# Performance work log

Hardware: AMD Instinct MI355X
Metric: run time of the kernel (lower is better)

## Reference

```python
import jax, jax.numpy as jnp
import numpy as np

HEAD_DIM = 16

def setup_inputs() -> dict:
    key = jax.random.key(0)
    ks = jax.random.split(key, 6)
    b, m, n, e, k, d = 2, 2048, 2048, 128, 8, HEAD_DIM
    # xavier-uniform-like scale for [e, d] fan
    s = float(np.sqrt(6.0 / (e + d)))
    return {
        "x": jax.random.normal(ks[0], (b, m, e), dtype=jnp.float32),
        "y": jax.random.normal(ks[1], (b, n, e), dtype=jnp.float32),
        "lambda1": jax.random.uniform(ks[2], (k, e, d), jnp.float32, -s, s),
        "lambda2": jax.random.uniform(ks[3], (k, e, d), jnp.float32, -s, s),
        "theta1": jax.random.uniform(ks[4], (k, e, d), jnp.float32, -s, s),
        "theta2": jax.random.uniform(ks[5], (k, e, d), jnp.float32, -s, s),
        "bias_lambda": jnp.zeros((k, d), jnp.float32),
        "bias_theta": jnp.zeros((k, d), jnp.float32),
    }

def reference(x, y, lambda1, lambda2, theta1, theta2, bias_lambda, bias_theta):
    head_dim = lambda1.shape[-1]
    # r: [b, m, k, d]
    r = jnp.einsum('bmp,kpd->bmkd', x, lambda1) + bias_lambda
    # dot_att: [k, b, m, n] (bilinear QK via per-head projections of x and y)
    dot_att = jnp.einsum('bmkd,kqd,bnq->kbmn', r, lambda2, y)
    dot_att = dot_att * (head_dim ** -0.5)
    # softmax over the query/m axis (-2), NOT the key axis
    att = jax.nn.softmax(dot_att, axis=-2)
    # combine: [b, n, k, d]
    r2 = jnp.einsum('kbmn,bmp,kpd->bnkd', att, x, theta1) + bias_theta
    # output: [b, n, emb_dim_x]
    return jnp.einsum('bnkd,kqd->bnq', r2, theta2)
```

## Files before the change

kernel.cpp:

```cpp
#include <hip/hip_runtime.h>
#include <math.h>

#define BB 2
#define MM 2048
#define NN 2048
#define EE 128
#define KH 8
#define DD 16
#define NHEADS (BB * KH)
#define MSPLIT 8
#define MCHUNK (MM / MSPLIT)
#define LOG2E 1.44269504088896340736f
#define QSCALE (0.25f * LOG2E)


typedef __bf16 bf16x8 __attribute__((ext_vector_type(8)));
typedef __bf16 bf16x4 __attribute__((ext_vector_type(4)));
typedef float  f32x16 __attribute__((ext_vector_type(16)));
typedef float  f32x4  __attribute__((ext_vector_type(4)));

__device__ inline bf16x8 cvt8(float4 a, float4 b) {
    bf16x8 r;
    r[0] = (__bf16)a.x; r[1] = (__bf16)a.y; r[2] = (__bf16)a.z; r[3] = (__bf16)a.w;
    r[4] = (__bf16)b.x; r[5] = (__bf16)b.y; r[6] = (__bf16)b.z; r[7] = (__bf16)b.w;
    return r;
}

__global__ __launch_bounds__(256) void proj_kernel(
    const float* __restrict__ x, const float* __restrict__ y,
    const float* __restrict__ lambda1, const float* __restrict__ lambda2,
    const float* __restrict__ theta1, const float* __restrict__ bias_lambda,
    __bf16* __restrict__ rK, __bf16* __restrict__ kyQ, __bf16* __restrict__ Vt)
{
    const int grp  = blockIdx.x;
    const int f    = blockIdx.y;
    const int head = blockIdx.z;
    const int b = head >> 3, kh = head & 7;
    const int wave = threadIdx.x >> 6;
    const int lane = threadIdx.x & 63;
    const int l15 = lane & 15, g4 = lane >> 4;

    const float* W   = ((f == 0) ? lambda1 : (f == 1) ? theta1 : lambda2)
                       + (size_t)kh * EE * DD;
    const float* src = ((f == 2) ? y : x) + (size_t)b * MM * EE;

    bf16x8 wf[4];
    #pragma unroll
    for (int kb = 0; kb < 4; ++kb) {
        const float* wp = W + (size_t)(32 * kb + 8 * g4) * DD + l15;
        bf16x8 t;
        #pragma unroll
        for (int e = 0; e < 8; ++e) t[e] = (__bf16)wp[e * DD];
        wf[kb] = t;
    }
    const float bl = (f == 0) ? bias_lambda[kh * DD + l15] : 0.f;

    const int m0 = (grp * 4 + wave) * 16;
    const float* xp = src + (size_t)(m0 + l15) * EE + 8 * g4;

    f32x4 acc;
    #pragma unroll
    for (int r = 0; r < 4; ++r) acc[r] = 0.f;

    #pragma unroll
    for (int kb = 0; kb < 4; ++kb) {
        float4 a = *(const float4*)(xp + 32 * kb);
        float4 c = *(const float4*)(xp + 32 * kb + 4);
        bf16x8 xf = cvt8(a, c);
        if (f == 1) acc = __builtin_amdgcn_mfma_f32_16x16x32_bf16(wf[kb], xf, acc, 0, 0, 0);
        else        acc = __builtin_amdgcn_mfma_f32_16x16x32_bf16(xf, wf[kb], acc, 0, 0, 0);
    }

    if (f == 0) {
        #pragma unroll
        for (int r = 0; r < 4; ++r)
            rK[((size_t)head * MM + m0 + 4 * g4 + r) * DD + l15] = (__bf16)(acc[r] + bl);
    } else if (f == 2) {
        #pragma unroll
        for (int r = 0; r < 4; ++r)
            kyQ[((size_t)head * NN + m0 + 4 * g4 + r) * DD + l15] = (__bf16)(acc[r] * QSCALE);
    } else {
        #pragma unroll
        for (int r = 0; r < 4; ++r)
            Vt[((size_t)head * DD + 4 * g4 + r) * MM + m0 + l15] = (__bf16)acc[r];
    }
}

__global__ __launch_bounds__(256) void attn_kernel(
    const __bf16* __restrict__ rK, const __bf16* __restrict__ kyQ,
    const __bf16* __restrict__ Vt,
    float* __restrict__ Opart, float* __restrict__ mlP)
{
    __shared__ __bf16 Pst[4][32][40];

    const int tid  = threadIdx.x;
    const int wave = tid >> 6;
    const int lane = tid & 63;
    const int head = blockIdx.x >> 4;
    const int nbase = (blockIdx.x & 15) * 128 + wave * 32;
    const int ms   = blockIdx.y;
    const int b = head >> 3, kh = head & 7;

    const int l31 = lane & 31;
    const int hi  = lane >> 5;
    const int l15 = lane & 15;
    const int g4  = lane >> 4;

    const bf16x8 qf = *reinterpret_cast<const bf16x8*>(
        kyQ + ((size_t)head * NN + nbase + l31) * DD + 8 * hi);

    f32x4 o0, o1;
    #pragma unroll
    for (int i = 0; i < 4; ++i) { o0[i] = 0.f; o1[i] = 0.f; }
    float lsum = 0.f;

    const __bf16* kb = rK + (size_t)head * MM * DD;
    const __bf16* vb = Vt + (size_t)head * DD * MM;

    #pragma unroll
    for (int it = 0; it < MCHUNK / 32; ++it) {
        const int m0 = ms * MCHUNK + it * 32;

        const bf16x8 kf = *reinterpret_cast<const bf16x8*>(
            kb + ((size_t)(m0 + l31)) * DD + 8 * hi);
        const bf16x8 vf = *reinterpret_cast<const bf16x8*>(
            vb + (size_t)l15 * MM + m0 + 8 * g4);

        f32x16 s;
        #pragma unroll
        for (int i = 0; i < 16; ++i) s[i] = 0.f;
        s = __builtin_amdgcn_mfma_f32_32x32x16_bf16(kf, qf, s, 0, 0, 0);

        #pragma unroll
        for (int r = 0; r < 16; ++r) { s[r] = exp2f(s[r]); lsum += s[r]; }

        #pragma unroll
        for (int qd = 0; qd < 4; ++qd) {
            bf16x4 pk;
            pk[0] = (__bf16)s[4 * qd + 0];
            pk[1] = (__bf16)s[4 * qd + 1];
            pk[2] = (__bf16)s[4 * qd + 2];
            pk[3] = (__bf16)s[4 * qd + 3];
            *reinterpret_cast<bf16x4*>(&Pst[wave][l31][8 * qd + 4 * hi]) = pk;
        }

        const bf16x8 pa0 = *reinterpret_cast<const bf16x8*>(&Pst[wave][l15][8 * g4]);
        const bf16x8 pa1 = *reinterpret_cast<const bf16x8*>(&Pst[wave][16 + l15][8 * g4]);

        o0 = __builtin_amdgcn_mfma_f32_16x16x32_bf16(pa0, vf, o0, 0, 0, 0);
        o1 = __builtin_amdgcn_mfma_f32_16x16x32_bf16(pa1, vf, o1, 0, 0, 0);
    }

    lsum += __shfl_xor(lsum, 32);

    float* obase = Opart + (((size_t)ms * BB + b) * NN) * (KH * DD) + kh * DD;
    #pragma unroll
    for (int r = 0; r < 4; ++r) {
        const int n0 = nbase + 4 * g4 + r;
        const int n1 = n0 + 16;
        obase[(size_t)n0 * (KH * DD) + l15] = o0[r];
        obase[(size_t)n1 * (KH * DD) + l15] = o1[r];
    }
    if (lane < 32) {
        mlP[(((size_t)ms * BB + b) * NN + nbase + l31) * KH + kh] = lsum;
    }
}

__global__ __launch_bounds__(256) void combine_kernel(
    const float* __restrict__ Opart, const float* __restrict__ mlP,
    const float* __restrict__ bias_theta, const float* __restrict__ theta2,
    float* __restrict__ out)
{
    __shared__ float r2s[4][128];

    const int blk = blockIdx.x;
    const int b   = blk >> 9;
    const int n0  = (blk & 511) * 4;
    const int tid = threadIdx.x;

    {
        const int n_loc = tid >> 6;
        const int k  = (tid >> 3) & 7;
        const int dh = tid & 7;
        const int n = n0 + n_loc;

        float L = 0.f;
        float2 O = make_float2(0.f, 0.f);
        #pragma unroll
        for (int s = 0; s < MSPLIT; ++s) {
            L += mlP[(((size_t)s * BB + b) * NN + n) * KH + k];
            const float2 op = *(const float2*)(
                Opart + (((size_t)s * BB + b) * NN + n) * (KH * DD) + k * DD + dh * 2);
            O.x += op.x;
            O.y += op.y;
        }
        const float inv = 1.f / L;
        const float* bt = bias_theta + k * DD + dh * 2;
        float2 res;
        res.x = fmaf(O.x, inv, bt[0]);
        res.y = fmaf(O.y, inv, bt[1]);
        *(float2*)&r2s[n_loc][k * DD + dh * 2] = res;
    }
    __syncthreads();
    {
        const int q   = tid & 127;
        const int nl0 = tid >> 7;
        float acc0 = 0.f, acc1 = 0.f;
        #pragma unroll
        for (int k = 0; k < KH; ++k) {
            const float4* t2 = (const float4*)(theta2 + ((size_t)k * EE + q) * DD);
            const float4* ra = (const float4*)&r2s[nl0][k * DD];
            const float4* rb = (const float4*)&r2s[nl0 + 2][k * DD];
            #pragma unroll
            for (int j = 0; j < 4; ++j) {
                const float4 t = t2[j];
                const float4 a = ra[j];
                const float4 bq = rb[j];
                acc0 = fmaf(a.x, t.x, acc0);  acc0 = fmaf(a.y, t.y, acc0);
                acc0 = fmaf(a.z, t.z, acc0);  acc0 = fmaf(a.w, t.w, acc0);
                acc1 = fmaf(bq.x, t.x, acc1); acc1 = fmaf(bq.y, t.y, acc1);
                acc1 = fmaf(bq.z, t.z, acc1); acc1 = fmaf(bq.w, t.w, acc1);
            }
        }
        out[((size_t)b * NN + n0 + nl0) * EE + q]     = acc0;
        out[((size_t)b * NN + n0 + nl0 + 2) * EE + q] = acc1;
    }
}

extern "C" void kernel_launch(void* const* d_in, const int* in_sizes, int n_in,
                              void* d_out, int out_size, void* d_ws, size_t ws_size,
                              hipStream_t stream) {
    const float* x           = (const float*)d_in[0];
    const float* y           = (const float*)d_in[1];
    const float* lambda1     = (const float*)d_in[2];
    const float* lambda2     = (const float*)d_in[3];
    const float* theta1      = (const float*)d_in[4];
    const float* theta2      = (const float*)d_in[5];
    const float* bias_lambda = (const float*)d_in[6];
    const float* bias_theta  = (const float*)d_in[7];
    float* out = (float*)d_out;

    char* w = (char*)d_ws;
    __bf16* rK  = (__bf16*)w;  w += (size_t)NHEADS * MM * DD * 2;
    __bf16* kyQ = (__bf16*)w;  w += (size_t)NHEADS * NN * DD * 2;
    __bf16* Vt  = (__bf16*)w;  w += (size_t)NHEADS * DD * MM * 2;
    float* Opart = (float*)w;  w += (size_t)MSPLIT * BB * NN * KH * DD * 4;
    float* mlP   = (float*)w;

    hipLaunchKernelGGL(proj_kernel, dim3(32, 3, 16), dim3(256), 0, stream,
                       x, y, lambda1, lambda2, theta1, bias_lambda, rK, kyQ, Vt);
    hipLaunchKernelGGL(attn_kernel, dim3(256, MSPLIT), dim3(256), 0, stream,
                       rK, kyQ, Vt, Opart, mlP);
    hipLaunchKernelGGL(combine_kernel, dim3(1024), dim3(256), 0, stream,
                       Opart, mlP, bias_theta, theta2, out);
}
```

Baseline: 110.8 us.

## Fuse K/V projections, halve M split, partially unroll attention loop

The projection kernel now computes the lambda1 and theta1 projections of x in the same block, so each x tile is loaded and converted to bf16 once instead of twice. The launch grid shrinks from three to two projection slices. The attention split along M is halved, so each block covers a longer M chunk and writes fewer partial results for combine to read. The attention loop is now partially unrolled and the exp-sum uses two accumulators to shorten the dependency chain. The cost is fewer attention blocks, which means less parallelism, plus higher register pressure in the fused projection.

```diff
diff --git a/kernel.cpp b/kernel.cpp
--- a/kernel.cpp
+++ b/kernel.cpp
@@ -8,7 +8,7 @@
 #define KH 8
 #define DD 16
 #define NHEADS (BB * KH)
-#define MSPLIT 8
+#define MSPLIT 4
 #define MCHUNK (MM / MSPLIT)
 #define LOG2E 1.44269504088896340736f
 #define QSCALE (0.25f * LOG2E)
@@ -40,49 +40,63 @@
     const int lane = threadIdx.x & 63;
     const int l15 = lane & 15, g4 = lane >> 4;
 
-    const float* W   = ((f == 0) ? lambda1 : (f == 1) ? theta1 : lambda2)
-                       + (size_t)kh * EE * DD;
-    const float* src = ((f == 2) ? y : x) + (size_t)b * MM * EE;
-
-    bf16x8 wf[4];
-    #pragma unroll
-    for (int kb = 0; kb < 4; ++kb) {
-        const float* wp = W + (size_t)(32 * kb + 8 * g4) * DD + l15;
-        bf16x8 t;
-        #pragma unroll
-        for (int e = 0; e < 8; ++e) t[e] = (__bf16)wp[e * DD];
-        wf[kb] = t;
-    }
-    const float bl = (f == 0) ? bias_lambda[kh * DD + l15] : 0.f;
-
     const int m0 = (grp * 4 + wave) * 16;
-    const float* xp = src + (size_t)(m0 + l15) * EE + 8 * g4;
-
-    f32x4 acc;
-    #pragma unroll
-    for (int r = 0; r < 4; ++r) acc[r] = 0.f;
-
-    #pragma unroll
-    for (int kb = 0; kb < 4; ++kb) {
-        float4 a = *(const float4*)(xp + 32 * kb);
-        float4 c = *(const float4*)(xp + 32 * kb + 4);
-        bf16x8 xf = cvt8(a, c);
-        if (f == 1) acc = __builtin_amdgcn_mfma_f32_16x16x32_bf16(wf[kb], xf, acc, 0, 0, 0);
-        else        acc = __builtin_amdgcn_mfma_f32_16x16x32_bf16(xf, wf[kb], acc, 0, 0, 0);
-    }
 
     if (f == 0) {
-        #pragma unroll
-        for (int r = 0; r < 4; ++r)
-            rK[((size_t)head * MM + m0 + 4 * g4 + r) * DD + l15] = (__bf16)(acc[r] + bl);
-    } else if (f == 2) {
+        bf16x8 wfK[4], wfV[4];
+        #pragma unroll
+        for (int kb = 0; kb < 4; ++kb) {
+            const float* wpK = lambda1 + (size_t)kh * EE * DD + (size_t)(32 * kb + 8 * g4) * DD + l15;
+            const float* wpV = theta1  + (size_t)kh * EE * DD + (size_t)(32 * kb + 8 * g4) * DD + l15;
+            bf16x8 tK, tV;
+            #pragma unroll
+            for (int e = 0; e < 8; ++e) { tK[e] = (__bf16)wpK[e * DD]; tV[e] = (__bf16)wpV[e * DD]; }
+            wfK[kb] = tK; wfV[kb] = tV;
+        }
+        const float bl = bias_lambda[kh * DD + l15];
+
+        const float* xp = x + (size_t)b * MM * EE + (size_t)(m0 + l15) * EE + 8 * g4;
+        f32x4 accK, accV;
+        #pragma unroll
+        for (int r = 0; r < 4; ++r) { accK[r] = 0.f; accV[r] = 0.f; }
+
+        #pragma unroll
+        for (int kb = 0; kb < 4; ++kb) {
+            float4 a = *(const float4*)(xp + 32 * kb);
+            float4 c = *(const float4*)(xp + 32 * kb + 4);
+            bf16x8 xf = cvt8(a, c);
+            accK = __builtin_amdgcn_mfma_f32_16x16x32_bf16(xf, wfK[kb], accK, 0, 0, 0);
+            accV = __builtin_amdgcn_mfma_f32_16x16x32_bf16(wfV[kb], xf, accV, 0, 0, 0);
+        }
+
+        #pragma unroll
+        for (int r = 0; r < 4; ++r) {
+            rK[((size_t)head * MM + m0 + 4 * g4 + r) * DD + l15] = (__bf16)(accK[r] + bl);
+            Vt[((size_t)head * DD + 4 * g4 + r) * MM + m0 + l15] = (__bf16)accV[r];
+        }
+    } else {
+        bf16x8 wf[4];
+        #pragma unroll
+        for (int kb = 0; kb < 4; ++kb) {
+            const float* wp = lambda2 + (size_t)kh * EE * DD + (size_t)(32 * kb + 8 * g4) * DD + l15;
+            bf16x8 t;
+            #pragma unroll
+            for (int e = 0; e < 8; ++e) t[e] = (__bf16)wp[e * DD];
+            wf[kb] = t;
+        }
+        const float* yp = y + (size_t)b * NN * EE + (size_t)(m0 + l15) * EE + 8 * g4;
+        f32x4 acc;
+        #pragma unroll
+        for (int r = 0; r < 4; ++r) acc[r] = 0.f;
+        #pragma unroll
+        for (int kb = 0; kb < 4; ++kb) {
+            float4 a = *(const float4*)(yp + 32 * kb);
+            float4 c = *(const float4*)(yp + 32 * kb + 4);
+            acc = __builtin_amdgcn_mfma_f32_16x16x32_bf16(cvt8(a, c), wf[kb], acc, 0, 0, 0);
+        }
         #pragma unroll
         for (int r = 0; r < 4; ++r)
             kyQ[((size_t)head * NN + m0 + 4 * g4 + r) * DD + l15] = (__bf16)(acc[r] * QSCALE);
-    } else {
-        #pragma unroll
-        for (int r = 0; r < 4; ++r)
-            Vt[((size_t)head * DD + 4 * g4 + r) * MM + m0 + l15] = (__bf16)acc[r];
     }
 }
 
@@ -112,12 +126,12 @@
     f32x4 o0, o1;
     #pragma unroll
     for (int i = 0; i < 4; ++i) { o0[i] = 0.f; o1[i] = 0.f; }
-    float lsum = 0.f;
+    float lsumA = 0.f, lsumB = 0.f;
 
     const __bf16* kb = rK + (size_t)head * MM * DD;
     const __bf16* vb = Vt + (size_t)head * DD * MM;
 
-    #pragma unroll
+    #pragma unroll 4
     for (int it = 0; it < MCHUNK / 32; ++it) {
         const int m0 = ms * MCHUNK + it * 32;
 
@@ -132,7 +146,10 @@
         s = __builtin_amdgcn_mfma_f32_32x32x16_bf16(kf, qf, s, 0, 0, 0);
 
         #pragma unroll
-        for (int r = 0; r < 16; ++r) { s[r] = exp2f(s[r]); lsum += s[r]; }
+        for (int r = 0; r < 16; r += 2) {
+            s[r]     = exp2f(s[r]);     lsumA += s[r];
+            s[r + 1] = exp2f(s[r + 1]); lsumB += s[r + 1];
+        }
 
         #pragma unroll
         for (int qd = 0; qd < 4; ++qd) {
@@ -151,6 +168,7 @@
         o1 = __builtin_amdgcn_mfma_f32_16x16x32_bf16(pa1, vf, o1, 0, 0, 0);
     }
 
+    float lsum = lsumA + lsumB;
     lsum += __shfl_xor(lsum, 32);
 
     float* obase = Opart + (((size_t)ms * BB + b) * NN) * (KH * DD) + kh * DD;
@@ -247,7 +265,7 @@
     float* Opart = (float*)w;  w += (size_t)MSPLIT * BB * NN * KH * DD * 4;
     float* mlP   = (float*)w;
 
-    hipLaunchKernelGGL(proj_kernel, dim3(32, 3, 16), dim3(256), 0, stream,
+    hipLaunchKernelGGL(proj_kernel, dim3(32, 2, 16), dim3(256), 0, stream,
                        x, y, lambda1, lambda2, theta1, bias_lambda, rK, kyQ, Vt);
     hipLaunchKernelGGL(attn_kernel, dim3(256, MSPLIT), dim3(256), 0, stream,
                        rK, kyQ, Vt, Opart, mlP);
```

After: 109.5 us. Within noise of the previous version (-1.1%).
